# Performance work log

Measured on AMD Instinct MI355X. Metric: run time of the kernel, lower is better.

The kernel has to match this reference:

```python
import jax, jax.numpy as jnp
import numpy as np

E, N, D, H = 500000, 100000, 8, 256
BN_EPS = 1e-5


def _batchnorm(x, gamma, beta):
    # BatchNorm1d in training mode: biased batch statistics over dim 0
    mu = jnp.mean(x, axis=0)
    var = jnp.var(x, axis=0)
    return (x - mu) * jax.lax.rsqrt(var + BN_EPS) * gamma + beta


def _encoder(x, W1, b1, gamma, beta, W2, b2):
    h = jax.nn.relu(x @ W1 + b1)
    h = _batchnorm(h, gamma, beta)
    return h @ W2 + b2


def setup_inputs() -> dict:
    key = jax.random.key(0)
    ks = jax.random.split(key, 24)
    s = 0.05  # weight init scale
    inp = {
        "edge_attr": jax.random.normal(ks[0], (E, D), dtype=jnp.float32),
        "node_features": jax.random.normal(ks[1], (N, D), dtype=jnp.float32),
        "edge_index": jax.random.randint(ks[2], (2, E), 0, N, dtype=jnp.int32),
        "e_W1": jax.random.normal(ks[3], (D, H)) * s,
        "e_b1": jax.random.normal(ks[4], (H,)) * s,
        "e_gamma": jnp.ones((H,), jnp.float32),
        "e_beta": jnp.zeros((H,), jnp.float32),
        "e_W2": jax.random.normal(ks[5], (H, H)) * s,
        "e_b2": jax.random.normal(ks[6], (H,)) * s,
        "n_W1": jax.random.normal(ks[7], (D, H)) * s,
        "n_b1": jax.random.normal(ks[8], (H,)) * s,
        "n_gamma": jnp.ones((H,), jnp.float32),
        "n_beta": jnp.zeros((H,), jnp.float32),
        "n_W2": jax.random.normal(ks[9], (H, H)) * s,
        "n_b2": jax.random.normal(ks[10], (H,)) * s,
        "Wv": jax.random.normal(ks[11], (H, H)) * s,
        "bv": jax.random.normal(ks[12], (H,)) * s,
        "Wo": jax.random.normal(ks[13], (H, H)) * s,
        "bo": jax.random.normal(ks[14], (H,)) * s,
        "Wp": jax.random.normal(ks[15], (H, D)) * s,
        "bp": jax.random.normal(ks[16], (D,)) * s,
    }
    return inp


def reference(edge_attr, node_features, edge_index,
              e_W1, e_b1, e_gamma, e_beta, e_W2, e_b2,
              n_W1, n_b1, n_gamma, n_beta, n_W2, n_b2,
              Wv, bv, Wo, bo, Wp, bp):
    # edge encoder: Linear -> ReLU -> BatchNorm1d -> Linear
    edge_encoded = _encoder(edge_attr, e_W1, e_b1, e_gamma, e_beta, e_W2, e_b2)

    # gather endpoint features and average (node dim == edge dim, slice is no-op)
    src = node_features[edge_index[0]]  # [E, D]
    tgt = node_features[edge_index[1]]  # [E, D]
    node_context = (src + tgt) * 0.5
    node_encoded = _encoder(node_context, n_W1, n_b1, n_gamma, n_beta, n_W2, n_b2)

    # MultiheadAttention with seq_len=1: softmax over one key is exactly 1,
    # so output = out_proj(v_proj(node_encoded)); q/k projections cancel.
    attn_out = (node_encoded @ Wv + bv) @ Wo + bo  # [E, H]

    edge_attr_enhanced = attn_out @ Wp + bp  # [E, D]
    return edge_attr + 0.5 * edge_attr_enhanced
```

## Files before the change

### kernel.cpp

```cpp
#include <hip/hip_runtime.h>
#include <hip/hip_bf16.h>
#include <string.h>

#define E_CNT 500000
#define N_CNT 100000
#define HID   256
#define NTILE 31250

typedef short short8 __attribute__((ext_vector_type(8)));
typedef float f32x4 __attribute__((ext_vector_type(4)));

__device__ __forceinline__ unsigned short f2bf(float f){
  union { float f; unsigned int i; } v; v.f = f;
  unsigned int u = v.i;
  u = u + 0x7FFFu + ((u >> 16) & 1u);
  return (unsigned short)(u >> 16);
}

__device__ __forceinline__ unsigned int pk_bf16(float a, float b){
  __hip_bfloat162 p = __float22bfloat162_rn(make_float2(a, b));
  unsigned int u; memcpy(&u, &p, 4); return u;
}

__device__ __forceinline__ void init_w1_lds(unsigned short* w1l,
                                            const float* W1, const float* b1,
                                            int tid){
  int ch = tid;
  #pragma unroll
  for (int j = 0; j < 8; ++j){
    unsigned short w = f2bf(W1[j * HID + ch]);
    w1l[ch * 24 + j]     = w;
    w1l[ch * 24 + 8 + j] = w;
  }
  w1l[ch * 24 + 16] = f2bf(2.0f * b1[ch]);
  #pragma unroll
  for (int j = 17; j < 24; ++j) w1l[ch * 24 + j] = 0;
  if (tid < 32) w1l[256 * 24 + tid] = 0;
}

__global__ __launch_bounds__(256, 3) void k1_stats(
    const int* __restrict__ eidx, const float* __restrict__ nf,
    const float* __restrict__ W1, const float* __restrict__ b1,
    float* __restrict__ part, float* __restrict__ bd2)
{
  __shared__ unsigned short w1l[256 * 24 + 32];
  __shared__ unsigned short ctx[4][16 * 40];
  __shared__ float sred[2][4][256];

  const int tid = threadIdx.x, lane = tid & 63, wid = tid >> 6;
  const int gw = blockIdx.x * 4 + wid, nw = gridDim.x * 4;
  const int m = lane & 15, q = lane >> 4;
  const int r = lane >> 2, side = (lane >> 1) & 1, half = lane & 1;

  if (blockIdx.x == 0 && tid < 16) bd2[tid] = 0.f;

  init_w1_lds(w1l, W1, b1, tid);

  unsigned short* myctx = ctx[wid];
  for (int i = lane; i < 16 * 40; i += 64) myctx[i] = 0;
  if (lane < 16) myctx[lane * 40 + 16] = 0x3F80;
  __syncthreads();

  const f32x4 z4 = {0.f, 0.f, 0.f, 0.f};
  f32x4 sacc[16], qacc[16];
  #pragma unroll
  for (int nt = 0; nt < 16; ++nt){ sacc[nt] = z4; qacc[nt] = z4; }

  int t = gw;
  float4 nfc = make_float4(0.f,0.f,0.f,0.f); int i1 = 0;
  if (t < NTILE){
    int id0 = eidx[side * E_CNT + t * 16 + r];
    nfc = ((const float4*)nf)[id0 * 2 + half];
  }
  { int tn = t + nw;
    if (tn < NTILE) i1 = eidx[side * E_CNT + tn * 16 + r]; }

  for (; t < NTILE; t += nw){
    *(uint2*)&myctx[r * 40 + side * 8 + half * 4] =
        make_uint2(pk_bf16(nfc.x, nfc.y), pk_bf16(nfc.z, nfc.w));

    int tn1 = t + nw, tn2 = t + 2 * nw;
    float4 nfn = make_float4(0.f,0.f,0.f,0.f); int i2 = 0;
    if (tn1 < NTILE) nfn = ((const float4*)nf)[i1 * 2 + half];
    if (tn2 < NTILE) i2 = eidx[side * E_CNT + tn2 * 16 + r];

    asm volatile("s_waitcnt lgkmcnt(0)" ::: "memory");
    short8 bfr = *(const short8*)&myctx[m * 40 + q * 8];
    #pragma unroll
    for (int nt = 0; nt < 16; ++nt){
      short8 afr = *(const short8*)&w1l[(nt * 16 + m) * 24 + q * 8];
      f32x4 c = __builtin_amdgcn_mfma_f32_16x16x32_bf16(afr, bfr, z4, 0, 0, 0);
      f32x4 hv = __builtin_elementwise_max(c, z4);
      sacc[nt] += hv;
      qacc[nt] += hv * hv;
    }
    nfc = nfn; i1 = i2;
  }

  #pragma unroll
  for (int nt = 0; nt < 16; ++nt){
    #pragma unroll
    for (int i = 0; i < 4; ++i){
      float v = sacc[nt][i], w = qacc[nt][i];
      v += __shfl_xor(v, 1); w += __shfl_xor(w, 1);
      v += __shfl_xor(v, 2); w += __shfl_xor(w, 2);
      v += __shfl_xor(v, 4); w += __shfl_xor(w, 4);
      v += __shfl_xor(v, 8); w += __shfl_xor(w, 8);
      if (m == 0){
        int j = nt * 16 + q * 4 + i;
        sred[0][wid][j] = v;
        sred[1][wid][j] = w;
      }
    }
  }
  __syncthreads();
  {
    int j = tid;
    float s0 = sred[0][0][j] + sred[0][1][j] + sred[0][2][j] + sred[0][3][j];
    float s1 = sred[1][0][j] + sred[1][1][j] + sred[1][2][j] + sred[1][3][j];
    part[blockIdx.x * 512 + j]       = s0;
    part[blockIdx.x * 512 + 256 + j] = s1;
  }
}

__global__ __launch_bounds__(256) void kchain(
    const float* __restrict__ part, int nb,
    const float* __restrict__ gamma, const float* __restrict__ beta,
    const float* __restrict__ Wo, const float* __restrict__ Wp,
    const float* __restrict__ Wv, const float* __restrict__ nW2,
    const float* __restrict__ bv, const float* __restrict__ bo,
    const float* __restrict__ bp, const float* __restrict__ nb2,
    unsigned short* __restrict__ wd2t, float* __restrict__ bd2)
{
  __shared__ float WpL[2048], T1L[2048], T2L[2048];
  __shared__ float scr[2048];
  __shared__ float stL[8];
  const int t = threadIdx.x, b = blockIdx.x;

  for (int i = t; i < 2048; i += 256) WpL[i] = Wp[i];

  {
    int cl = t >> 6, i = t & 63;
    int c = b * 4 + cl;
    float s0 = 0.f, s1 = 0.f;
    for (int b2 = i; b2 < nb; b2 += 64){
      s0 += part[b2 * 512 + c];
      s1 += part[b2 * 512 + 256 + c];
    }
    scr[cl * 128 + i]      = s0;
    scr[cl * 128 + 64 + i] = s1;
  }
  __syncthreads();
  if (t < 4){
    float s0 = 0.f, s1 = 0.f;
    for (int i = 0; i < 64; ++i){
      s0 += scr[t * 128 + i];
      s1 += scr[t * 128 + 64 + i];
    }
    const float invE = 1.0f / (float)E_CNT;
    float mu  = s0 * invE;
    float var = fmaxf(s1 * invE - mu * mu, 0.f);
    float s   = gamma[b * 4 + t] * rsqrtf(var + 4.0f * 1e-5f);
    stL[t]     = s;
    stL[4 + t] = beta[b * 4 + t] - mu * s;
  }
  __syncthreads();

  float acc[8];
  #pragma unroll
  for (int d = 0; d < 8; ++d) acc[d] = 0.f;
  for (int jb = 0; jb < 64; ++jb){
    float4 w4 = ((const float4*)(Wo + t * HID))[jb];
    float wv4[4] = {w4.x, w4.y, w4.z, w4.w};
    #pragma unroll
    for (int dj = 0; dj < 4; ++dj){
      int j = jb * 4 + dj;
      #pragma unroll
      for (int d = 0; d < 8; ++d) acc[d] = fmaf(wv4[dj], WpL[j * 8 + d], acc[d]);
    }
  }
  #pragma unroll
  for (int d = 0; d < 8; ++d) T1L[t * 8 + d] = acc[d];
  __syncthreads();

  #pragma unroll
  for (int d = 0; d < 8; ++d) acc[d] = 0.f;
  for (int jb = 0; jb < 64; ++jb){
    float4 w4 = ((const float4*)(Wv + t * HID))[jb];
    float wv4[4] = {w4.x, w4.y, w4.z, w4.w};
    #pragma unroll
    for (int dj = 0; dj < 4; ++dj){
      int j = jb * 4 + dj;
      #pragma unroll
      for (int d = 0; d < 8; ++d) acc[d] = fmaf(wv4[dj], T1L[j * 8 + d], acc[d]);
    }
  }
  #pragma unroll
  for (int d = 0; d < 8; ++d) T2L[t * 8 + d] = acc[d];
  __syncthreads();

  {
    int cl = t >> 6, d = (t >> 3) & 7, p8 = t & 7;
    int c = b * 4 + cl;
    const float* row = nW2 + c * HID;
    float a = 0.f;
    for (int j = p8 * 32; j < p8 * 32 + 32; ++j)
      a = fmaf(row[j], T2L[j * 8 + d], a);
    scr[t] = a;
  }
  __syncthreads();
  {
    int cl = t >> 6, d = (t >> 3) & 7, p8 = t & 7;
    if (p8 == 0){
      float w = 0.f;
      #pragma unroll
      for (int i = 0; i < 8; ++i) w += scr[t + i];
      int c = b * 4 + cl;
      wd2t[d * HID + c]       = f2bf(0.5f * stL[cl] * w);
      wd2t[(8 + d) * HID + c] = 0;
      scr[1024 + cl * 8 + d]  = stL[4 + cl] * w;
    }
  }
  __syncthreads();
  if (t < 8){
    float a = scr[1024 + t] + scr[1024 + 8 + t] +
              scr[1024 + 16 + t] + scr[1024 + 24 + t];
    if (b == 0){
      float s2 = bp[t];
      for (int j = 0; j < HID; ++j){
        s2 = fmaf(nb2[j], T2L[j * 8 + t], s2);
        s2 = fmaf(bv[j],  T1L[j * 8 + t], s2);
        s2 = fmaf(bo[j],  WpL[j * 8 + t], s2);
      }
      a += s2;
    }
    atomicAdd(&bd2[t], a);
  }
}

__global__ __launch_bounds__(256, 3) void k3_main(
    const int* __restrict__ eidx, const float* __restrict__ nf,
    const float* __restrict__ ea,
    const float* __restrict__ W1, const float* __restrict__ b1,
    const unsigned short* __restrict__ wd2t, const float* __restrict__ bd2,
    float* __restrict__ out)
{
  __shared__ unsigned short w1l[256 * 24 + 32];
  __shared__ unsigned short ctx[4][16 * 40];
  __shared__ unsigned short hbuf[4][16 * 264];

  const int tid = threadIdx.x, lane = tid & 63, wid = tid >> 6;
  const int gw = blockIdx.x * 4 + wid, ngw = gridDim.x * 4;
  const int m = lane & 15, q = lane >> 4;
  const int r = lane >> 2, side = (lane >> 1) & 1, half = lane & 1;

  init_w1_lds(w1l, W1, b1, tid);

  short8 w2fr[8];
  #pragma unroll
  for (int kb = 0; kb < 8; ++kb)
    w2fr[kb] = *(const short8*)&wd2t[m * HID + kb * 32 + q * 8];
  const float bd2v = (m < 8) ? 0.5f * bd2[m] : 0.f;

  unsigned short* myctx = ctx[wid];
  unsigned short* myh   = hbuf[wid];
  for (int i = lane; i < 16 * 40; i += 64) myctx[i] = 0;
  if (lane < 16) myctx[lane * 40 + 16] = 0x3F80;
  __syncthreads();

  const f32x4 z4 = {0.f, 0.f, 0.f, 0.f};

  int t = gw;
  float4 nfc = make_float4(0.f,0.f,0.f,0.f); int i1 = 0;
  if (t < NTILE){
    int id0 = eidx[side * E_CNT + t * 16 + r];
    nfc = ((const float4*)nf)[id0 * 2 + half];
  }
  { int tn = t + ngw;
    if (tn < NTILE) i1 = eidx[side * E_CNT + tn * 16 + r]; }

  const bool dok = (m < 8);
  for (; t < NTILE; t += ngw){
    *(uint2*)&myctx[r * 40 + side * 8 + half * 4] =
        make_uint2(pk_bf16(nfc.x, nfc.y), pk_bf16(nfc.z, nfc.w));

    float eav[4];
    #pragma unroll
    for (int i = 0; i < 4; ++i)
      eav[i] = dok ? ea[(t * 16 + q * 4 + i) * 8 + m] : 0.f;

    int tn1 = t + ngw, tn2 = t + 2 * ngw;
    float4 nfn = make_float4(0.f,0.f,0.f,0.f); int i2 = 0;
    if (tn1 < NTILE) nfn = ((const float4*)nf)[i1 * 2 + half];
    if (tn2 < NTILE) i2 = eidx[side * E_CNT + tn2 * 16 + r];

    asm volatile("s_waitcnt lgkmcnt(0)" ::: "memory");
    short8 bfr = *(const short8*)&myctx[m * 40 + q * 8];
    #pragma unroll
    for (int nt = 0; nt < 16; ++nt){
      short8 afr = *(const short8*)&w1l[(nt * 16 + m) * 24 + q * 8];
      f32x4 c = __builtin_amdgcn_mfma_f32_16x16x32_bf16(afr, bfr, z4, 0, 0, 0);
      f32x4 hv = __builtin_elementwise_max(c, z4);
      *(uint2*)&myh[m * 264 + nt * 16 + q * 4] =
          make_uint2(pk_bf16(hv[0], hv[1]), pk_bf16(hv[2], hv[3]));
    }
    asm volatile("s_waitcnt lgkmcnt(0)" ::: "memory");
    f32x4 acc = z4;
    #pragma unroll
    for (int kb = 0; kb < 8; ++kb){
      short8 afr = *(const short8*)&myh[m * 264 + kb * 32 + q * 8];
      acc = __builtin_amdgcn_mfma_f32_16x16x32_bf16(afr, w2fr[kb], acc, 0, 0, 0);
    }
    if (dok){
      #pragma unroll
      for (int i = 0; i < 4; ++i){
        float o = eav[i] + acc[i] + bd2v;
        out[(t * 16 + q * 4 + i) * 8 + m] = o;
      }
    }
    nfc = nfn; i1 = i2;
  }
}

extern "C" void kernel_launch(void* const* d_in, const int* in_sizes, int n_in,
                              void* d_out, int out_size, void* d_ws, size_t ws_size,
                              hipStream_t stream)
{
  const float* ea   = (const float*)d_in[0];
  const float* nf   = (const float*)d_in[1];
  const int*   eidx = (const int*)d_in[2];
  const float* nW1    = (const float*)d_in[9];
  const float* nb1    = (const float*)d_in[10];
  const float* ngamma = (const float*)d_in[11];
  const float* nbeta  = (const float*)d_in[12];
  const float* nW2    = (const float*)d_in[13];
  const float* nb2    = (const float*)d_in[14];
  const float* Wv     = (const float*)d_in[15];
  const float* bv     = (const float*)d_in[16];
  const float* Wo     = (const float*)d_in[17];
  const float* bo     = (const float*)d_in[18];
  const float* Wp     = (const float*)d_in[19];
  const float* bp     = (const float*)d_in[20];

  long avail = (long)ws_size - 8192 - 64;
  int nb = (int)(avail / 2048);
  if (nb > 768) nb = 768;
  if (nb < 1)   nb = 1;

  char* ws = (char*)d_ws;
  float* ws_part          = (float*)(ws + 0);
  unsigned short* ws_wd2t = (unsigned short*)(ws + (size_t)nb * 2048);
  float* ws_bd2           = (float*)(ws + (size_t)nb * 2048 + 8192);

  k1_stats<<<dim3(nb), dim3(256), 0, stream>>>(eidx, nf, nW1, nb1,
                                               ws_part, ws_bd2);
  kchain<<<dim3(64), dim3(256), 0, stream>>>(
      ws_part, nb, ngamma, nbeta, Wo, Wp, Wv, nW2, bv, bo, bp, nb2,
      ws_wd2t, ws_bd2);
  k3_main<<<dim3(768), dim3(256), 0, stream>>>(
      eidx, nf, ea, nW1, nb1, ws_wd2t, ws_bd2, (float*)d_out);
}
```

Before: 218.4 us.

## Split weight-chain GEMVs into parallel kernels and cache W1 fragments in registers

The serial Wo·Wp and Wv·T1 products, which kchain recomputed redundantly in each of its 64 blocks, move into two small row-parallel kernels (256 blocks of 64 threads with a wave-level shuffle reduction). The results go to workspace, and the bias-fold loop is spread across blocks instead of running on block 0 alone. Both heavy kernels now load their W1 MFMA fragments into registers once rather than reading LDS on every tile. This trades redundant per-block work for two extra kernel launches, and the 16 short8 register fragments raise VGPR pressure, which could cut occupancy under launch_bounds(256,3).

```diff
diff --git a/kernel.cpp b/kernel.cpp
--- a/kernel.cpp
+++ b/kernel.cpp
@@ -61,6 +61,11 @@
   if (lane < 16) myctx[lane * 40 + 16] = 0x3F80;
   __syncthreads();
 
+  short8 w1fr[16];
+  #pragma unroll
+  for (int nt = 0; nt < 16; ++nt)
+    w1fr[nt] = *(const short8*)&w1l[(nt * 16 + m) * 24 + q * 8];
+
   const f32x4 z4 = {0.f, 0.f, 0.f, 0.f};
   f32x4 sacc[16], qacc[16];
   #pragma unroll
@@ -88,8 +93,7 @@
     short8 bfr = *(const short8*)&myctx[m * 40 + q * 8];
     #pragma unroll
     for (int nt = 0; nt < 16; ++nt){
-      short8 afr = *(const short8*)&w1l[(nt * 16 + m) * 24 + q * 8];
-      f32x4 c = __builtin_amdgcn_mfma_f32_16x16x32_bf16(afr, bfr, z4, 0, 0, 0);
+      f32x4 c = __builtin_amdgcn_mfma_f32_16x16x32_bf16(w1fr[nt], bfr, z4, 0, 0, 0);
       f32x4 hv = __builtin_elementwise_max(c, z4);
       sacc[nt] += hv;
       qacc[nt] += hv * hv;
@@ -123,21 +127,54 @@
   }
 }
 
-__global__ __launch_bounds__(256) void kchain(
+__global__ __launch_bounds__(64) void kRow(const float* __restrict__ W,
+                                           const float* __restrict__ X,
+                                           float* __restrict__ Y)
+{
+  const int r = blockIdx.x, t = threadIdx.x;
+  float4 w4 = ((const float4*)(W + r * HID))[t];
+  float wv[4] = {w4.x, w4.y, w4.z, w4.w};
+  float acc[8];
+  #pragma unroll
+  for (int d = 0; d < 8; ++d) acc[d] = 0.f;
+  #pragma unroll
+  for (int dj = 0; dj < 4; ++dj){
+    int j = 4 * t + dj;
+    float4 x0 = ((const float4*)(X + j * 8))[0];
+    float4 x1 = ((const float4*)(X + j * 8))[1];
+    acc[0] = fmaf(wv[dj], x0.x, acc[0]); acc[1] = fmaf(wv[dj], x0.y, acc[1]);
+    acc[2] = fmaf(wv[dj], x0.z, acc[2]); acc[3] = fmaf(wv[dj], x0.w, acc[3]);
+    acc[4] = fmaf(wv[dj], x1.x, acc[4]); acc[5] = fmaf(wv[dj], x1.y, acc[5]);
+    acc[6] = fmaf(wv[dj], x1.z, acc[6]); acc[7] = fmaf(wv[dj], x1.w, acc[7]);
+  }
+  #pragma unroll
+  for (int d = 0; d < 8; ++d){
+    acc[d] += __shfl_xor(acc[d], 1);
+    acc[d] += __shfl_xor(acc[d], 2);
+    acc[d] += __shfl_xor(acc[d], 4);
+    acc[d] += __shfl_xor(acc[d], 8);
+    acc[d] += __shfl_xor(acc[d], 16);
+    acc[d] += __shfl_xor(acc[d], 32);
+  }
+  if (t < 8) Y[r * 8 + t] = acc[t];
+}
+
+__global__ __launch_bounds__(256) void kC(
     const float* __restrict__ part, int nb,
     const float* __restrict__ gamma, const float* __restrict__ beta,
-    const float* __restrict__ Wo, const float* __restrict__ Wp,
-    const float* __restrict__ Wv, const float* __restrict__ nW2,
+    const float* __restrict__ nW2,
+    const float* __restrict__ T1s, const float* __restrict__ T2s,
+    const float* __restrict__ Wp,
     const float* __restrict__ bv, const float* __restrict__ bo,
     const float* __restrict__ bp, const float* __restrict__ nb2,
     unsigned short* __restrict__ wd2t, float* __restrict__ bd2)
 {
-  __shared__ float WpL[2048], T1L[2048], T2L[2048];
+  __shared__ float T2L[2048];
   __shared__ float scr[2048];
   __shared__ float stL[8];
   const int t = threadIdx.x, b = blockIdx.x;
 
-  for (int i = t; i < 2048; i += 256) WpL[i] = Wp[i];
+  for (int i = t; i < 2048; i += 256) T2L[i] = T2s[i];
 
   {
     int cl = t >> 6, i = t & 63;
@@ -164,39 +201,6 @@
     stL[t]     = s;
     stL[4 + t] = beta[b * 4 + t] - mu * s;
   }
-  __syncthreads();
-
-  float acc[8];
-  #pragma unroll
-  for (int d = 0; d < 8; ++d) acc[d] = 0.f;
-  for (int jb = 0; jb < 64; ++jb){
-    float4 w4 = ((const float4*)(Wo + t * HID))[jb];
-    float wv4[4] = {w4.x, w4.y, w4.z, w4.w};
-    #pragma unroll
-    for (int dj = 0; dj < 4; ++dj){
-      int j = jb * 4 + dj;
-      #pragma unroll
-      for (int d = 0; d < 8; ++d) acc[d] = fmaf(wv4[dj], WpL[j * 8 + d], acc[d]);
-    }
-  }
-  #pragma unroll
-  for (int d = 0; d < 8; ++d) T1L[t * 8 + d] = acc[d];
-  __syncthreads();
-
-  #pragma unroll
-  for (int d = 0; d < 8; ++d) acc[d] = 0.f;
-  for (int jb = 0; jb < 64; ++jb){
-    float4 w4 = ((const float4*)(Wv + t * HID))[jb];
-    float wv4[4] = {w4.x, w4.y, w4.z, w4.w};
-    #pragma unroll
-    for (int dj = 0; dj < 4; ++dj){
-      int j = jb * 4 + dj;
-      #pragma unroll
-      for (int d = 0; d < 8; ++d) acc[d] = fmaf(wv4[dj], T1L[j * 8 + d], acc[d]);
-    }
-  }
-  #pragma unroll
-  for (int d = 0; d < 8; ++d) T2L[t * 8 + d] = acc[d];
   __syncthreads();
 
   {
@@ -225,15 +229,14 @@
   if (t < 8){
     float a = scr[1024 + t] + scr[1024 + 8 + t] +
               scr[1024 + 16 + t] + scr[1024 + 24 + t];
-    if (b == 0){
-      float s2 = bp[t];
-      for (int j = 0; j < HID; ++j){
-        s2 = fmaf(nb2[j], T2L[j * 8 + t], s2);
-        s2 = fmaf(bv[j],  T1L[j * 8 + t], s2);
-        s2 = fmaf(bo[j],  WpL[j * 8 + t], s2);
-      }
-      a += s2;
-    }
+    #pragma unroll
+    for (int jj = 0; jj < 4; ++jj){
+      int j = 4 * b + jj;
+      a = fmaf(nb2[j], T2L[j * 8 + t], a);
+      a = fmaf(bv[j],  T1s[j * 8 + t], a);
+      a = fmaf(bo[j],  Wp[j * 8 + t], a);
+    }
+    if (b == 0) a += bp[t];
     atomicAdd(&bd2[t], a);
   }
 }
@@ -268,6 +271,11 @@
   if (lane < 16) myctx[lane * 40 + 16] = 0x3F80;
   __syncthreads();
 
+  short8 w1fr[16];
+  #pragma unroll
+  for (int nt = 0; nt < 16; ++nt)
+    w1fr[nt] = *(const short8*)&w1l[(nt * 16 + m) * 24 + q * 8];
+
   const f32x4 z4 = {0.f, 0.f, 0.f, 0.f};
 
   int t = gw;
@@ -298,8 +306,7 @@
     short8 bfr = *(const short8*)&myctx[m * 40 + q * 8];
     #pragma unroll
     for (int nt = 0; nt < 16; ++nt){
-      short8 afr = *(const short8*)&w1l[(nt * 16 + m) * 24 + q * 8];
-      f32x4 c = __builtin_amdgcn_mfma_f32_16x16x32_bf16(afr, bfr, z4, 0, 0, 0);
+      f32x4 c = __builtin_amdgcn_mfma_f32_16x16x32_bf16(w1fr[nt], bfr, z4, 0, 0, 0);
       f32x4 hv = __builtin_elementwise_max(c, z4);
       *(uint2*)&myh[m * 264 + nt * 16 + q * 4] =
           make_uint2(pk_bf16(hv[0], hv[1]), pk_bf16(hv[2], hv[3]));
@@ -342,20 +349,25 @@
   const float* Wp     = (const float*)d_in[19];
   const float* bp     = (const float*)d_in[20];
 
-  long avail = (long)ws_size - 8192 - 64;
+  long avail = (long)ws_size - 8192 - 64 - 16384;
   int nb = (int)(avail / 2048);
   if (nb > 768) nb = 768;
   if (nb < 1)   nb = 1;
 
   char* ws = (char*)d_ws;
+  size_t off = (size_t)nb * 2048;
   float* ws_part          = (float*)(ws + 0);
-  unsigned short* ws_wd2t = (unsigned short*)(ws + (size_t)nb * 2048);
-  float* ws_bd2           = (float*)(ws + (size_t)nb * 2048 + 8192);
+  unsigned short* ws_wd2t = (unsigned short*)(ws + off);
+  float* ws_bd2           = (float*)(ws + off + 8192);
+  float* ws_t1            = (float*)(ws + off + 8192 + 64);
+  float* ws_t2            = (float*)(ws + off + 8192 + 64 + 8192);
 
   k1_stats<<<dim3(nb), dim3(256), 0, stream>>>(eidx, nf, nW1, nb1,
                                                ws_part, ws_bd2);
-  kchain<<<dim3(64), dim3(256), 0, stream>>>(
-      ws_part, nb, ngamma, nbeta, Wo, Wp, Wv, nW2, bv, bo, bp, nb2,
+  kRow<<<dim3(256), dim3(64), 0, stream>>>(Wo, Wp, ws_t1);
+  kRow<<<dim3(256), dim3(64), 0, stream>>>(Wv, ws_t1, ws_t2);
+  kC<<<dim3(64), dim3(256), 0, stream>>>(
+      ws_part, nb, ngamma, nbeta, nW2, ws_t1, ws_t2, Wp, bv, bo, bp, nb2,
       ws_wd2t, ws_bd2);
   k3_main<<<dim3(768), dim3(256), 0, stream>>>(
       eidx, nf, ea, nW1, nb1, ws_wd2t, ws_bd2, (float*)d_out);
```

New measurement: 249.8 us. +14.4%, slower.
